# Optimization experiments

Measured on AMD Instinct MI355X. Metric: run time of the kernel, lower is better.

Reference implementation:

```python
import jax, jax.numpy as jnp
import numpy as np

B, C, MID, OUT, T, N = 8, 128, 64, 128, 4, 512


def setup_inputs() -> dict:
    key = jax.random.key(0)
    ks = jax.random.split(key, 5)
    def w(k, o, i, scale):
        return (jax.random.normal(k, (o, i), jnp.float32) * scale)
    return {
        "pc": jax.random.normal(ks[0], (B, C, T, N), jnp.float32),
        "theta_w": w(ks[1], MID, C, 0.05), "theta_b": jnp.zeros((MID,), jnp.float32),
        "phi_w": w(ks[2], MID, C, 0.05), "phi_b": jnp.zeros((MID,), jnp.float32),
        "g_w": w(ks[3], MID, C, 0.05), "g_b": jnp.zeros((MID,), jnp.float32),
        "refine_w": w(ks[4], OUT, MID, 0.05), "refine_b": jnp.zeros((OUT,), jnp.float32),
    }


def reference(pc, theta_w, theta_b, phi_w, phi_b, g_w, g_b, refine_w, refine_b):
    b, c, t, n = pc.shape
    tn = t * n
    # pt_utils.Conv2d with bn=False: 1x1 conv + bias + ReLU
    def proj(wt, bs):
        h = jnp.einsum('oc,bctn->botn', wt, pc) + bs[None, :, None, None]
        return jax.nn.relu(h).reshape(b, -1, tn)  # [B, mid, TN]

    theta = proj(theta_w, theta_b).transpose(0, 2, 1)  # [B, TN, mid]
    phi = proj(phi_w, phi_b)                            # [B, mid, TN]
    g = proj(g_w, g_b).transpose(0, 2, 1)               # [B, TN, mid]

    scores = jnp.einsum('bqm,bmk->bqk', theta, phi)     # [B, TN, TN]
    corr = jax.nn.softmax(scores, axis=1)               # softmax over QUERY axis (dim=1)
    y = jnp.einsum('bqk,bkm->bmq', corr, g)             # bmm then transpose(1,2): [B, mid, TN]

    # pt_utils.Conv1d with bn=False: 1x1 conv + bias + ReLU
    refined = jax.nn.relu(jnp.einsum('om,bmq->boq', refine_w, y) + refine_b[None, :, None])
    # faithful raw reshape (row-major, same as torch) then permute, plus residual
    z = refined.reshape(b, t, n, -1).transpose(0, 3, 1, 2) + pc
    return z
```

## Files before the change

kernel.cpp:

```cpp
#include <hip/hip_runtime.h>


constexpr int NL75_TN  = 2048;
constexpr int NL75_MID = 64;
constexpr int NL75_C   = 128;

typedef __attribute__((ext_vector_type(8))) short nl75_bf8;
typedef __attribute__((ext_vector_type(4))) float nl75_f4;

__device__ __forceinline__ unsigned short nl75_f2b(float f) {
  unsigned x = __float_as_uint(f);
  return (unsigned short)((x + 0x7fffu + ((x >> 16) & 1u)) >> 16);
}

__device__ __forceinline__ unsigned int nl75_pkbf16(float lo, float hi) {
  unsigned int r;
  asm("v_cvt_pk_bf16_f32 %0, %1, %2" : "=v"(r) : "v"(lo), "v"(hi));
  return r;
}

typedef const __attribute__((address_space(1))) unsigned int* nl75_gp;
typedef __attribute__((address_space(3))) unsigned int* nl75_lp;
__device__ __forceinline__ void nl75_gld16(const void* g, void* l) {
  __builtin_amdgcn_global_load_lds((nl75_gp)g, (nl75_lp)l, 16, 0, 0);
}

__device__ __forceinline__ void nl75_stage64(const unsigned short* src,
                                             size_t pitch, unsigned short* lds,
                                             int tid) {
  const int w = tid >> 6, lane = tid & 63;
#pragma unroll
  for (int r = 0; r < 2; r++) {
    const int slot = r * 256 + w * 64 + lane;
    const int row = slot >> 3, x = slot & 7;
    const unsigned short* s =
        src + (size_t)row * pitch + ((x * 8) ^ ((row & 7) << 3));
    nl75_gld16(s, lds + (size_t)(r * 256 + w * 64) * 8);
  }
}

__global__ void NonLocalLayer_75771813036638_kernel() {}

__global__ void nl75_proj(const float* pc, const float* w0, const float* b0,
                          const float* w1, const float* b1, const float* w2,
                          const float* b2, unsigned short* thT,
                          unsigned short* phT, unsigned short* gN, int bOff,
                          int nb) {
  __shared__ float wT[NL75_C][68];
  const int bl = blockIdx.x, pj = blockIdx.y, qt = blockIdx.z;
  const int b = bOff + bl;
  const float* wp = (pj == 0) ? w0 : (pj == 1) ? w1 : w2;
  const float* bp = (pj == 0) ? b0 : (pj == 1) ? b1 : b2;
  const int tid = threadIdx.x;
  for (int i = tid; i < NL75_MID * NL75_C; i += 256)
    wT[i & 127][i >> 7] = wp[i];
  __syncthreads();
  const int lq = tid & 63, mg = tid >> 6;
  const int q = qt * 64 + lq, m0 = mg * 16;
  const float* pcb = pc + (long long)b * NL75_C * NL75_TN + q;
  float acc[16];
#pragma unroll
  for (int i = 0; i < 16; i++) acc[i] = bp[m0 + i];
  for (int c = 0; c < NL75_C; c++) {
    float p = pcb[(long long)c * NL75_TN];
#pragma unroll
    for (int i = 0; i < 16; i++) acc[i] = fmaf(wT[c][m0 + i], p, acc[i]);
  }
  if (pj < 2) {
    unsigned int u[8];
#pragma unroll
    for (int i = 0; i < 8; i++)
      u[i] = nl75_pkbf16(fmaxf(acc[2 * i], 0.0f), fmaxf(acc[2 * i + 1], 0.0f));
    unsigned short* dst =
        (pj == 0 ? thT : phT) + ((size_t)bl * NL75_TN + q) * 64 + m0;
    *reinterpret_cast<uint4*>(dst) = *reinterpret_cast<uint4*>(&u[0]);
    *reinterpret_cast<uint4*>(dst + 8) = *reinterpret_cast<uint4*>(&u[4]);
  } else {
#pragma unroll
    for (int i = 0; i < 16; i++)
      gN[((size_t)bl * NL75_MID + m0 + i) * NL75_TN + q] =
          nl75_f2b(fmaxf(acc[i], 0.0f));
  }
}

__global__ void nl75_stats(const unsigned short* thT, const unsigned short* phT,
                           float* Mp, float* Sp, int nb, int qsplit) {
  __shared__ unsigned short thL[2][64 * 64];
  const int bl = blockIdx.x;
  const int kt = blockIdx.y & 31, qs = blockIdx.y >> 5;
  const int tid = threadIdx.x, lane = tid & 63, w = tid >> 6;
  const int l15 = lane & 15, quad = lane >> 4;
  const int k0 = kt * 64;
  const unsigned short* thB = thT + (size_t)bl * NL75_TN * 64;
  const unsigned short* phB = phT + (size_t)bl * NL75_TN * 64;
  const size_t kr = (size_t)(k0 + w * 16 + l15) * 64;
  const nl75_bf8 b0 = *(const nl75_bf8*)&phB[kr + quad * 8];
  const nl75_bf8 b1 = *(const nl75_bf8*)&phB[kr + 32 + quad * 8];
  const int qtN = 32 / qsplit, qtBeg = qs * qtN;
  nl75_stage64(thB + (size_t)(qtBeg * 64) * 64, 64, thL[0], tid);
  __syncthreads();
  float M = -1e30f, S = 0.0f;
  for (int qt = qtBeg; qt < qtBeg + qtN; qt++) {
    const int cur = (qt - qtBeg) & 1;
    if (qt + 1 < qtBeg + qtN)
      nl75_stage64(thB + (size_t)((qt + 1) * 64) * 64, 64, thL[cur ^ 1], tid);
#pragma unroll
    for (int q16 = 0; q16 < 4; q16++) {
      const int qr = q16 * 16 + l15;
      const int sw = (qr & 7) << 3;
      const nl75_bf8 a0 = *(const nl75_bf8*)&thL[cur][qr * 64 + ((quad * 8) ^ sw)];
      const nl75_bf8 a1 =
          *(const nl75_bf8*)&thL[cur][qr * 64 + ((32 + quad * 8) ^ sw)];
      nl75_f4 c = {0.0f, 0.0f, 0.0f, 0.0f};
      c = __builtin_amdgcn_mfma_f32_16x16x32_bf16(a0, b0, c, 0, 0, 0);
      c = __builtin_amdgcn_mfma_f32_16x16x32_bf16(a1, b1, c, 0, 0, 0);
      float mx = fmaxf(fmaxf(c[0], c[1]), fmaxf(c[2], c[3]));
      float nM = fmaxf(M, mx);
      float sum = __expf(c[0] - nM) + __expf(c[1] - nM) + __expf(c[2] - nM) +
                  __expf(c[3] - nM);
      S = S * __expf(M - nM) + sum;
      M = nM;
    }
    __syncthreads();
  }
#pragma unroll
  for (int off = 16; off <= 32; off <<= 1) {
    float Mo = __shfl_xor(M, off);
    float So = __shfl_xor(S, off);
    float nM = fmaxf(M, Mo);
    S = S * __expf(M - nM) + So * __expf(Mo - nM);
    M = nM;
  }
  if (quad == 0) {
    const long long base = ((long long)(qs * nb + bl)) * NL75_TN + k0;
    Mp[base + w * 16 + l15] = M;
    Sp[base + w * 16 + l15] = S;
  }
}

__global__ void nl75_sred(const float* Mp, const float* Sp, float* mW,
                          float* izW, int nb, int qsplit) {
  const int bl = blockIdx.x;
  const int k = blockIdx.y * 256 + threadIdx.x;
  float M = -1e30f;
  for (int qs = 0; qs < qsplit; qs++)
    M = fmaxf(M, Mp[((size_t)(qs * nb + bl)) * NL75_TN + k]);
  float S = 0.0f;
  for (int qs = 0; qs < qsplit; qs++) {
    size_t idx = ((size_t)(qs * nb + bl)) * NL75_TN + k;
    S += Sp[idx] * __expf(Mp[idx] - M);
  }
  mW[(size_t)bl * NL75_TN + k] = M;
  izW[(size_t)bl * NL75_TN + k] = 1.0f / S;
}

__global__ void nl75_attn(const unsigned short* thT, const unsigned short* phT,
                          const unsigned short* gN, const float* mW,
                          const float* izW, float* yPart, int nb, int ksplit) {
  __shared__ unsigned short phL[2][64 * 64];
  __shared__ unsigned short gL[2][64 * 64];
  const int wg = blockIdx.x;
  const int bl = wg % nb;
  const int rest = wg / nb;
  const int qt = rest & 15, ks = rest >> 4;
  const int tid = threadIdx.x, lane = tid & 63, w = tid >> 6;
  const int l15 = lane & 15, quad = lane >> 4;
  const int q0 = qt * 128;
  const unsigned short* thB = thT + (size_t)bl * NL75_TN * 64;
  const unsigned short* phB = phT + (size_t)bl * NL75_TN * 64;
  const unsigned short* gB = gN + (size_t)bl * NL75_MID * NL75_TN;
  const float* mB = mW + (size_t)bl * NL75_TN;
  const float* izB = izW + (size_t)bl * NL75_TN;
  const int ktN = 32 / ksplit;
  const int ktBeg = ks * ktN, ktEnd = ktBeg + ktN;
  nl75_stage64(phB + (size_t)(ktBeg * 64) * 64, 64, phL[0], tid);
  nl75_stage64(gB + ktBeg * 64, NL75_TN, gL[0], tid);
  nl75_bf8 aq[2][2];
#pragma unroll
  for (int s = 0; s < 2; s++) {
    const size_t qr = (size_t)(q0 + s * 64 + w * 16 + l15) * 64;
    aq[s][0] = *(const nl75_bf8*)&thB[qr + quad * 8];
    aq[s][1] = *(const nl75_bf8*)&thB[qr + 32 + quad * 8];
  }
  nl75_f4 yacc[2][4];
#pragma unroll
  for (int s = 0; s < 2; s++)
#pragma unroll
    for (int i = 0; i < 4; i++) yacc[s][i] = (nl75_f4){0.0f, 0.0f, 0.0f, 0.0f};
  __syncthreads();
  union Frag { nl75_bf8 h; unsigned int u[4]; };
  for (int kt = ktBeg; kt < ktEnd; kt++) {
    const int cur = (kt - ktBeg) & 1;
    const int k0 = kt * 64;
    if (kt + 1 < ktEnd) {
      nl75_stage64(phB + (size_t)((kt + 1) * 64) * 64, 64, phL[cur ^ 1], tid);
      nl75_stage64(gB + (kt + 1) * 64, NL75_TN, gL[cur ^ 1], tid);
    }
    unsigned int pk[2][8];
#pragma unroll
    for (int t = 0; t < 4; t++) {
      const int krr = t * 16 + l15;
      const int sw = (krr & 7) << 3;
      const nl75_bf8 b0 =
          *(const nl75_bf8*)&phL[cur][krr * 64 + ((quad * 8) ^ sw)];
      const nl75_bf8 b1 =
          *(const nl75_bf8*)&phL[cur][krr * 64 + ((32 + quad * 8) ^ sw)];
      const nl75_f4 mk = *(const nl75_f4*)&mB[k0 + t * 16 + quad * 4];
      const nl75_f4 zk = *(const nl75_f4*)&izB[k0 + t * 16 + quad * 4];
#pragma unroll
      for (int s = 0; s < 2; s++) {
        nl75_f4 c = {0.0f, 0.0f, 0.0f, 0.0f};
        c = __builtin_amdgcn_mfma_f32_16x16x32_bf16(b0, aq[s][0], c, 0, 0, 0);
        c = __builtin_amdgcn_mfma_f32_16x16x32_bf16(b1, aq[s][1], c, 0, 0, 0);
        pk[s][t * 2 + 0] = nl75_pkbf16(__expf(c[0] - mk[0]) * zk[0],
                                       __expf(c[1] - mk[1]) * zk[1]);
        pk[s][t * 2 + 1] = nl75_pkbf16(__expf(c[2] - mk[2]) * zk[2],
                                       __expf(c[3] - mk[3]) * zk[3]);
      }
    }
#pragma unroll
    for (int mtile = 0; mtile < 4; mtile++) {
      const int m = mtile * 16 + l15;
      const int sw = (m & 7) << 3;
      const unsigned short* row = &gL[cur][m * 64];
      Frag bg0, bg1;
      *(uint2*)&bg0.u[0] = *(const uint2*)&row[(quad * 4) ^ sw];
      *(uint2*)&bg0.u[2] = *(const uint2*)&row[(16 + quad * 4) ^ sw];
      *(uint2*)&bg1.u[0] = *(const uint2*)&row[(32 + quad * 4) ^ sw];
      *(uint2*)&bg1.u[2] = *(const uint2*)&row[(48 + quad * 4) ^ sw];
#pragma unroll
      for (int s = 0; s < 2; s++) {
        Frag a0, a1;
        a0.u[0] = pk[s][0]; a0.u[1] = pk[s][1];
        a0.u[2] = pk[s][2]; a0.u[3] = pk[s][3];
        a1.u[0] = pk[s][4]; a1.u[1] = pk[s][5];
        a1.u[2] = pk[s][6]; a1.u[3] = pk[s][7];
        yacc[s][mtile] = __builtin_amdgcn_mfma_f32_16x16x32_bf16(
            a0.h, bg0.h, yacc[s][mtile], 0, 0, 0);
        yacc[s][mtile] = __builtin_amdgcn_mfma_f32_16x16x32_bf16(
            a1.h, bg1.h, yacc[s][mtile], 0, 0, 0);
      }
    }
    __syncthreads();
  }
  float* yB = yPart + ((size_t)(ks * nb + bl) * NL75_MID) * NL75_TN;
#pragma unroll
  for (int s = 0; s < 2; s++)
#pragma unroll
    for (int mtile = 0; mtile < 4; mtile++) {
      float4 v = make_float4(yacc[s][mtile][0], yacc[s][mtile][1],
                             yacc[s][mtile][2], yacc[s][mtile][3]);
      *(float4*)&yB[(size_t)(mtile * 16 + l15) * NL75_TN + q0 + s * 64 +
                    w * 16 + quad * 4] = v;
    }
}

__global__ void nl75_yred(const float* yPart, float* y, int nb, int ksplit) {
  const size_t tot = (size_t)nb * NL75_MID * NL75_TN / 4;
  const size_t stride = tot;
  const float4* src = (const float4*)yPart;
  float4* dst = (float4*)y;
  for (size_t i = (size_t)blockIdx.x * 256 + threadIdx.x; i < tot;
       i += (size_t)gridDim.x * 256) {
    float4 a = src[i];
    for (int ks = 1; ks < ksplit; ks++) {
      float4 b = src[(size_t)ks * stride + i];
      a.x += b.x; a.y += b.y; a.z += b.z; a.w += b.w;
    }
    dst[i] = a;
  }
}

__global__ void nl75_refsc(const float* yPart, const float* rW,
                           const float* rB, const float* pc, float* outP,
                           int bOff, int nb, int ksplit) {
  __shared__ float rwS[32][66];
  __shared__ float yS[NL75_MID][132];
  const int bl = blockIdx.x, cg = blockIdx.y, t = blockIdx.z;
  const int b = bOff + bl, c0 = cg * 8, tid = threadIdx.x;
  for (int i = tid; i < 32 * NL75_MID; i += 256) {
    int oh = i >> 6, m = i & 63;
    rwS[oh][m] = rW[(long long)(t * 32 + oh) * NL75_MID + m];
  }
  for (int i = tid; i < NL75_MID * 128; i += 256) {
    int m = i >> 7, qi = i & 127;
    int i16 = qi >> 3, cl = qi & 7;
    long long off = (long long)m * NL75_TN + i16 * 128 + c0 + cl;
    float v = 0.0f;
    for (int ks = 0; ks < ksplit; ks++)
      v += yPart[((long long)(ks * nb + bl) * NL75_MID) * NL75_TN + off];
    yS[m][qi] = v;
  }
  __syncthreads();
  const int oh0 = (tid >> 5) * 4;
  const int q4 = (tid & 31) * 4;
  float acc[4][4];
#pragma unroll
  for (int i = 0; i < 4; i++) {
    float bias = rB[t * 32 + oh0 + i];
#pragma unroll
    for (int j = 0; j < 4; j++) acc[i][j] = bias;
  }
  for (int m = 0; m < NL75_MID; m++) {
    float yv[4];
#pragma unroll
    for (int j = 0; j < 4; j++) yv[j] = yS[m][q4 + j];
#pragma unroll
    for (int i = 0; i < 4; i++) {
      float w = rwS[oh0 + i][m];
#pragma unroll
      for (int j = 0; j < 4; j++) acc[i][j] = fmaf(w, yv[j], acc[i][j]);
    }
  }
#pragma unroll
  for (int i = 0; i < 4; i++) {
    int oh = oh0 + i;
#pragma unroll
    for (int j = 0; j < 4; j++) {
      int qi = q4 + j;
      int i16 = qi >> 3, cl = qi & 7;
      int n = oh * 16 + i16;
      long long idx = (((long long)b * 128 + c0 + cl) * 4 + t) * 512 + n;
      outP[idx] = fmaxf(acc[i][j], 0.0f) + pc[idx];
    }
  }
}

extern "C" void kernel_launch(void* const* d_in, const int* in_sizes, int n_in,
                              void* d_out, int out_size, void* d_ws, size_t ws_size,
                              hipStream_t stream) {
  const float* pc = (const float*)d_in[0];
  const float* tw = (const float*)d_in[1];
  const float* tb = (const float*)d_in[2];
  const float* pw = (const float*)d_in[3];
  const float* pb = (const float*)d_in[4];
  const float* gw = (const float*)d_in[5];
  const float* gb = (const float*)d_in[6];
  const float* rw = (const float*)d_in[7];
  const float* rb = (const float*)d_in[8];
  float* out = (float*)d_out;

  const size_t yPB = (size_t)NL75_MID * NL75_TN;
  const size_t bfB8 = 3ull * 8 * NL75_TN * 64 * 2;
  const size_t base8 = bfB8 + 2ull * 8 * NL75_TN * 4;
  auto need = [&](int qs, int ks, int yr) -> size_t {
    return base8 + (2ull * qs * 8 * NL75_TN + (size_t)ks * 8 * yPB +
                    (size_t)yr * 8 * yPB) * 4;
  };
  const size_t needMid = base8 + 8ull * yPB * 4;

  int nb, qsplit, ksplit;
  bool alias, yred;
  if (ws_size >= need(8, 8, 1)) {
    nb = 8; qsplit = 8; ksplit = 8; alias = false; yred = true;
  } else if (ws_size >= need(8, 4, 1)) {
    nb = 8; qsplit = 8; ksplit = 4; alias = false; yred = true;
  } else if (ws_size >= need(4, 4, 1)) {
    nb = 8; qsplit = 4; ksplit = 4; alias = false; yred = true;
  } else if (ws_size >= need(4, 4, 0)) {
    nb = 8; qsplit = 4; ksplit = 4; alias = false; yred = false;
  } else if (ws_size >= needMid) {
    nb = 8; qsplit = 1; ksplit = 1; alias = true; yred = false;
  } else {
    nb = 1; qsplit = 1; ksplit = 1; alias = true; yred = false;
  }
  const int nloop = 8 / nb;

  unsigned short* thT = (unsigned short*)d_ws;
  unsigned short* phT = thT + (size_t)nb * NL75_TN * 64;
  unsigned short* gN = phT + (size_t)nb * NL75_TN * 64;
  float* mW = (float*)(gN + (size_t)nb * NL75_MID * NL75_TN);
  float* izW = mW + (size_t)nb * NL75_TN;
  float *Mp, *Sp, *yPart, *yFull;
  if (alias) {
    Mp = mW; Sp = izW;
    yPart = izW + (size_t)nb * NL75_TN;
    yFull = yPart;
  } else {
    Mp = izW + (size_t)nb * NL75_TN;
    Sp = Mp + (size_t)qsplit * nb * NL75_TN;
    yPart = Sp + (size_t)qsplit * nb * NL75_TN;
    yFull = yPart + (size_t)ksplit * nb * yPB;
  }

  for (int l = 0; l < nloop; l++) {
    const int bOff = l * nb;
    nl75_proj<<<dim3(nb, 3, 32), 256, 0, stream>>>(pc, tw, tb, pw, pb, gw, gb,
                                                   thT, phT, gN, bOff, nb);
    nl75_stats<<<dim3(nb, 32 * qsplit), 256, 0, stream>>>(thT, phT, Mp, Sp,
                                                          nb, qsplit);
    nl75_sred<<<dim3(nb, 8), 256, 0, stream>>>(Mp, Sp, mW, izW, nb, qsplit);
    nl75_attn<<<dim3(16 * ksplit * nb), 256, 0, stream>>>(thT, phT, gN, mW,
                                                          izW, yPart, nb,
                                                          ksplit);
    if (yred) {
      nl75_yred<<<dim3(1024), 256, 0, stream>>>(yPart, yFull, nb, ksplit);
      nl75_refsc<<<dim3(nb, 16, 4), 256, 0, stream>>>(yFull, rw, rb, pc, out,
                                                      bOff, nb, 1);
    } else {
      nl75_refsc<<<dim3(nb, 16, 4), 256, 0, stream>>>(yPart, rw, rb, pc, out,
                                                      bOff, nb, ksplit);
    }
  }
}
```

Baseline: 158.4 us.

## Fold softmax normalizer into exp2 offset, set wave priority, coalesce refine stores

```diff
diff --git a/kernel.cpp b/kernel.cpp
--- a/kernel.cpp
+++ b/kernel.cpp
@@ -4,6 +4,7 @@
 constexpr int NL75_TN  = 2048;
 constexpr int NL75_MID = 64;
 constexpr int NL75_C   = 128;
+constexpr float NL75_L2E = 1.4426950408889634f;
 
 typedef __attribute__((ext_vector_type(8))) short nl75_bf8;
 typedef __attribute__((ext_vector_type(4))) float nl75_f4;
@@ -16,6 +17,12 @@
 __device__ __forceinline__ unsigned int nl75_pkbf16(float lo, float hi) {
   unsigned int r;
   asm("v_cvt_pk_bf16_f32 %0, %1, %2" : "=v"(r) : "v"(lo), "v"(hi));
+  return r;
+}
+
+__device__ __forceinline__ float nl75_exp2(float x) {
+  float r;
+  asm("v_exp_f32 %0, %1" : "=v"(r) : "v"(x));
   return r;
 }
 
@@ -104,6 +111,7 @@
     const int cur = (qt - qtBeg) & 1;
     if (qt + 1 < qtBeg + qtN)
       nl75_stage64(thB + (size_t)((qt + 1) * 64) * 64, 64, thL[cur ^ 1], tid);
+    __builtin_amdgcn_s_setprio(1);
 #pragma unroll
     for (int q16 = 0; q16 < 4; q16++) {
       const int qr = q16 * 16 + l15;
@@ -121,6 +129,7 @@
       S = S * __expf(M - nM) + sum;
       M = nM;
     }
+    __builtin_amdgcn_s_setprio(0);
     __syncthreads();
   }
 #pragma unroll
@@ -138,8 +147,8 @@
   }
 }
 
-__global__ void nl75_sred(const float* Mp, const float* Sp, float* mW,
-                          float* izW, int nb, int qsplit) {
+__global__ void nl75_sred(const float* Mp, const float* Sp, float* ekW, int nb,
+                          int qsplit) {
   const int bl = blockIdx.x;
   const int k = blockIdx.y * 256 + threadIdx.x;
   float M = -1e30f;
@@ -150,13 +159,12 @@
     size_t idx = ((size_t)(qs * nb + bl)) * NL75_TN + k;
     S += Sp[idx] * __expf(Mp[idx] - M);
   }
-  mW[(size_t)bl * NL75_TN + k] = M;
-  izW[(size_t)bl * NL75_TN + k] = 1.0f / S;
+  ekW[(size_t)bl * NL75_TN + k] = M * NL75_L2E + __log2f(S);
 }
 
 __global__ void nl75_attn(const unsigned short* thT, const unsigned short* phT,
-                          const unsigned short* gN, const float* mW,
-                          const float* izW, float* yPart, int nb, int ksplit) {
+                          const unsigned short* gN, const float* ekW,
+                          float* yPart, int nb, int ksplit) {
   __shared__ unsigned short phL[2][64 * 64];
   __shared__ unsigned short gL[2][64 * 64];
   const int wg = blockIdx.x;
@@ -169,8 +177,7 @@
   const unsigned short* thB = thT + (size_t)bl * NL75_TN * 64;
   const unsigned short* phB = phT + (size_t)bl * NL75_TN * 64;
   const unsigned short* gB = gN + (size_t)bl * NL75_MID * NL75_TN;
-  const float* mB = mW + (size_t)bl * NL75_TN;
-  const float* izB = izW + (size_t)bl * NL75_TN;
+  const float* ekB = ekW + (size_t)bl * NL75_TN;
   const int ktN = 32 / ksplit;
   const int ktBeg = ks * ktN, ktEnd = ktBeg + ktN;
   nl75_stage64(phB + (size_t)(ktBeg * 64) * 64, 64, phL[0], tid);
@@ -196,6 +203,11 @@
       nl75_stage64(phB + (size_t)((kt + 1) * 64) * 64, 64, phL[cur ^ 1], tid);
       nl75_stage64(gB + (kt + 1) * 64, NL75_TN, gL[cur ^ 1], tid);
     }
+    nl75_f4 ek[4];
+#pragma unroll
+    for (int t = 0; t < 4; t++)
+      ek[t] = *(const nl75_f4*)&ekB[k0 + t * 16 + quad * 4];
+    __builtin_amdgcn_s_setprio(1);
     unsigned int pk[2][8];
 #pragma unroll
     for (int t = 0; t < 4; t++) {
@@ -205,17 +217,17 @@
           *(const nl75_bf8*)&phL[cur][krr * 64 + ((quad * 8) ^ sw)];
       const nl75_bf8 b1 =
           *(const nl75_bf8*)&phL[cur][krr * 64 + ((32 + quad * 8) ^ sw)];
-      const nl75_f4 mk = *(const nl75_f4*)&mB[k0 + t * 16 + quad * 4];
-      const nl75_f4 zk = *(const nl75_f4*)&izB[k0 + t * 16 + quad * 4];
 #pragma unroll
       for (int s = 0; s < 2; s++) {
         nl75_f4 c = {0.0f, 0.0f, 0.0f, 0.0f};
         c = __builtin_amdgcn_mfma_f32_16x16x32_bf16(b0, aq[s][0], c, 0, 0, 0);
         c = __builtin_amdgcn_mfma_f32_16x16x32_bf16(b1, aq[s][1], c, 0, 0, 0);
-        pk[s][t * 2 + 0] = nl75_pkbf16(__expf(c[0] - mk[0]) * zk[0],
-                                       __expf(c[1] - mk[1]) * zk[1]);
-        pk[s][t * 2 + 1] = nl75_pkbf16(__expf(c[2] - mk[2]) * zk[2],
-                                       __expf(c[3] - mk[3]) * zk[3]);
+        pk[s][t * 2 + 0] =
+            nl75_pkbf16(nl75_exp2(fmaf(c[0], NL75_L2E, -ek[t][0])),
+                        nl75_exp2(fmaf(c[1], NL75_L2E, -ek[t][1])));
+        pk[s][t * 2 + 1] =
+            nl75_pkbf16(nl75_exp2(fmaf(c[2], NL75_L2E, -ek[t][2])),
+                        nl75_exp2(fmaf(c[3], NL75_L2E, -ek[t][3])));
       }
     }
 #pragma unroll
@@ -241,6 +253,7 @@
             a1.h, bg1.h, yacc[s][mtile], 0, 0, 0);
       }
     }
+    __builtin_amdgcn_s_setprio(0);
     __syncthreads();
   }
   float* yB = yPart + ((size_t)(ks * nb + bl) * NL75_MID) * NL75_TN;
@@ -271,9 +284,9 @@
   }
 }
 
-__global__ void nl75_refsc(const float* yPart, const float* rW,
-                           const float* rB, const float* pc, float* outP,
-                           int bOff, int nb, int ksplit) {
+__global__ void nl75_refsc(const float* yIn, const float* rW, const float* rB,
+                           const float* pc, float* outP, int bOff, int nb,
+                           int ksplit) {
   __shared__ float rwS[32][66];
   __shared__ float yS[NL75_MID][132];
   const int bl = blockIdx.x, cg = blockIdx.y, t = blockIdx.z;
@@ -282,14 +295,25 @@
     int oh = i >> 6, m = i & 63;
     rwS[oh][m] = rW[(long long)(t * 32 + oh) * NL75_MID + m];
   }
-  for (int i = tid; i < NL75_MID * 128; i += 256) {
-    int m = i >> 7, qi = i & 127;
-    int i16 = qi >> 3, cl = qi & 7;
-    long long off = (long long)m * NL75_TN + i16 * 128 + c0 + cl;
-    float v = 0.0f;
-    for (int ks = 0; ks < ksplit; ks++)
-      v += yPart[((long long)(ks * nb + bl) * NL75_MID) * NL75_TN + off];
-    yS[m][qi] = v;
+  if (ksplit == 1) {
+    const float* yB0 = yIn + (size_t)bl * NL75_MID * NL75_TN;
+    for (int i = tid; i < NL75_MID * 32; i += 256) {
+      int m = i >> 5, r = i & 31;
+      int i16 = r >> 1, half = r & 1;
+      const float4 v = *(const float4*)&yB0[(size_t)m * NL75_TN + i16 * 128 +
+                                            c0 + half * 4];
+      *(float4*)&yS[m][i16 * 8 + half * 4] = v;
+    }
+  } else {
+    for (int i = tid; i < NL75_MID * 128; i += 256) {
+      int m = i >> 7, qi = i & 127;
+      int i16 = qi >> 3, cl = qi & 7;
+      long long off = (long long)m * NL75_TN + i16 * 128 + c0 + cl;
+      float v = 0.0f;
+      for (int ks = 0; ks < ksplit; ks++)
+        v += yIn[((long long)(ks * nb + bl) * NL75_MID) * NL75_TN + off];
+      yS[m][qi] = v;
+    }
   }
   __syncthreads();
   const int oh0 = (tid >> 5) * 4;
@@ -312,17 +336,29 @@
       for (int j = 0; j < 4; j++) acc[i][j] = fmaf(w, yv[j], acc[i][j]);
     }
   }
+  __syncthreads();
+  float* outS = &yS[0][0];
+  const int NP = 516;
 #pragma unroll
   for (int i = 0; i < 4; i++) {
-    int oh = oh0 + i;
+    const int oh = oh0 + i;
 #pragma unroll
     for (int j = 0; j < 4; j++) {
-      int qi = q4 + j;
-      int i16 = qi >> 3, cl = qi & 7;
-      int n = oh * 16 + i16;
-      long long idx = (((long long)b * 128 + c0 + cl) * 4 + t) * 512 + n;
-      outP[idx] = fmaxf(acc[i][j], 0.0f) + pc[idx];
-    }
+      const int qi = q4 + j;
+      outS[(qi & 7) * NP + oh * 16 + (qi >> 3)] = fmaxf(acc[i][j], 0.0f);
+    }
+  }
+  __syncthreads();
+  const size_t obase = (((size_t)b * 128 + c0) * 4 + t) * 512;
+#pragma unroll
+  for (int ii = 0; ii < 4; ii++) {
+    const int fi = ii * 256 + tid;
+    const int cl = fi >> 7, n0 = (fi & 127) * 4;
+    float4 v = *(const float4*)&outS[cl * NP + n0];
+    const size_t gi = obase + (size_t)cl * 4 * 512 + n0;
+    const float4 p = *(const float4*)&pc[gi];
+    v.x += p.x; v.y += p.y; v.z += p.z; v.w += p.w;
+    *(float4*)&outP[gi] = v;
   }
 }
 
@@ -369,15 +405,15 @@
   unsigned short* thT = (unsigned short*)d_ws;
   unsigned short* phT = thT + (size_t)nb * NL75_TN * 64;
   unsigned short* gN = phT + (size_t)nb * NL75_TN * 64;
-  float* mW = (float*)(gN + (size_t)nb * NL75_MID * NL75_TN);
-  float* izW = mW + (size_t)nb * NL75_TN;
+  float* s1 = (float*)(gN + (size_t)nb * NL75_MID * NL75_TN);
+  float* ekW = s1 + (size_t)nb * NL75_TN;
   float *Mp, *Sp, *yPart, *yFull;
   if (alias) {
-    Mp = mW; Sp = izW;
-    yPart = izW + (size_t)nb * NL75_TN;
+    Mp = s1; Sp = ekW;
+    yPart = ekW + (size_t)nb * NL75_TN;
     yFull = yPart;
   } else {
-    Mp = izW + (size_t)nb * NL75_TN;
+    Mp = ekW + (size_t)nb * NL75_TN;
     Sp = Mp + (size_t)qsplit * nb * NL75_TN;
     yPart = Sp + (size_t)qsplit * nb * NL75_TN;
     yFull = yPart + (size_t)ksplit * nb * yPB;
@@ -389,10 +425,9 @@
                                                    thT, phT, gN, bOff, nb);
     nl75_stats<<<dim3(nb, 32 * qsplit), 256, 0, stream>>>(thT, phT, Mp, Sp,
                                                           nb, qsplit);
-    nl75_sred<<<dim3(nb, 8), 256, 0, stream>>>(Mp, Sp, mW, izW, nb, qsplit);
-    nl75_attn<<<dim3(16 * ksplit * nb), 256, 0, stream>>>(thT, phT, gN, mW,
-                                                          izW, yPart, nb,
-                                                          ksplit);
+    nl75_sred<<<dim3(nb, 8), 256, 0, stream>>>(Mp, Sp, ekW, nb, qsplit);
+    nl75_attn<<<dim3(16 * ksplit * nb), 256, 0, stream>>>(thT, phT, gN, ekW,
+                                                          yPart, nb, ksplit);
     if (yred) {
       nl75_yred<<<dim3(1024), 256, 0, stream>>>(yPart, yFull, nb, ksplit);
       nl75_refsc<<<dim3(nb, 16, 4), 256, 0, stream>>>(yFull, rw, rb, pc, out,
```

Result: faster. 144.2 us (-9.0%).
